# Optimization experiments

Hardware: AMD Instinct MI355X
Metric: run time of the kernel (lower is better)

Reference implementation:

```python
import jax, jax.numpy as jnp
import numpy as np
import itertools, math

METRIC = [1.0, 1.0, 1.0]  # Cl(3,0)
EPS = 1e-6
SQRT2 = math.sqrt(2.0)


def _build_algebra(metric):
    d = len(metric)
    # basis blades ordered by grade, then lexicographic combination (repo convention)
    blades = []
    for g in range(d + 1):
        for c in itertools.combinations(range(d), g):
            blades.append(sum(1 << i for i in c))
    idx = {m: i for i, m in enumerate(blades)}
    n = len(blades)
    C = np.zeros((n, n, n), dtype=np.float32)  # cayley[i, j, k]: e_i * e_k -> sign * e_j
    for ia, am in enumerate(blades):
        for ik, bm in enumerate(blades):
            a = am >> 1
            swaps = 0
            while a:
                swaps += bin(a & bm).count('1')
                a >>= 1
            sign = -1.0 if (swaps & 1) else 1.0
            for i in range(d):
                if am & bm & (1 << i):
                    sign *= metric[i]
            C[ia, idx[am ^ bm], ik] = sign
    grades = np.array([bin(m).count('1') for m in blades])
    subspaces = np.array([int((grades == g).sum()) for g in range(d + 1)])
    paths = np.zeros((d + 1, d + 1, d + 1), dtype=bool)
    for i in range(d + 1):
        for j in range(d + 1):
            for k in range(d + 1):
                paths[i, j, k] = np.any(C[np.ix_(grades == i, grades == j, grades == k)] != 0)
    return C, subspaces, paths, grades

CAYLEY_NP, SUBSPACES, PATHS, GRADE_OF_COMP = _build_algebra(METRIC)
REP_IDX = np.repeat(np.arange(len(SUBSPACES)), SUBSPACES)  # component -> grade, len 8
PI, PJ, PK = np.nonzero(PATHS)                              # 20 active grade triples
ONEHOT_GRADE = np.eye(len(SUBSPACES), dtype=np.float32)[GRADE_OF_COMP]  # [8,4]

B, N_IN, N_OUT = 1024, 256, 256
DIM_MV = CAYLEY_NP.shape[0]  # 8
N_PATHS = int(PATHS.sum())   # 20


def mv_linear(x, w, bias=None):
    # MVLinear: per-grade weight repeated over components; einsum 'bm...i,nmi->bn...i'
    wr = w[:, :, REP_IDX]                       # [out, in, 8]
    out = jnp.einsum('bmi,nmi->bni', x, wr)
    if bias is not None:
        out = out.at[:, :, 0].add(bias[:, :, 0])  # bias embedded in scalar (grade-0) slot
    return out


def normalize_mv(x, a):
    # per-grade norms (Euclidean metric => L2 norm of each grade block)
    oh = jnp.asarray(ONEHOT_GRADE)
    norms = jnp.sqrt(jnp.einsum('bni,ig->bng', x * x, oh))  # [b, n, 4]
    interp = jax.nn.sigmoid(a)[None] * (norms - 1.0) + 1.0  # learned interp toward unit norm
    return x / (interp[:, :, REP_IDX] + EPS)


def gp_kernel(gp_weight):
    # scatter 20 path weights into (m, n, 4, 4, 4), repeat per subspace, mask by cayley
    m, n, _ = gp_weight.shape
    g = len(SUBSPACES)
    w4 = jnp.zeros((m, n, g, g, g), gp_weight.dtype).at[:, :, PI, PJ, PK].set(gp_weight)
    wrep = w4[:, :, REP_IDX][:, :, :, REP_IDX][:, :, :, :, REP_IDX]  # [m, n, 8, 8, 8]
    return jnp.asarray(CAYLEY_NP)[None, None] * wrep


def setup_inputs() -> dict:
    key = jax.random.key(0)
    ks = jax.random.split(key, 5)
    std_gp = 1.0 / math.sqrt(N_IN * (len(METRIC) + 1))
    std_lin = 1.0 / math.sqrt(N_IN)
    return {
        'x': jax.random.normal(ks[0], (B, N_IN, DIM_MV), jnp.float32),
        'w_right': jax.random.normal(ks[1], (N_IN, N_IN, len(SUBSPACES)), jnp.float32) * std_lin,
        'w_left': jax.random.normal(ks[2], (N_OUT, N_IN, len(SUBSPACES)), jnp.float32) * std_lin,
        'b_left': jax.random.normal(ks[3], (1, N_OUT, 1), jnp.float32) * 0.02,
        'norm_a': jnp.zeros((N_IN, len(SUBSPACES)), jnp.float32),  # normalization_init = 0
        'gp_weight': jax.random.normal(ks[4], (N_OUT, N_IN, N_PATHS), jnp.float32) * std_gp,
    }


def reference(x, w_right, w_left, b_left, norm_a, gp_weight):
    x_right = normalize_mv(mv_linear(x, w_right), norm_a)
    kernel = gp_kernel(gp_weight)                 # [m, n, 8, 8, 8]
    outer = jnp.einsum('bni,bnk->bnik', x, x_right)  # [b, n, 8, 8]
    prod = jnp.einsum('bnik,mnijk->bmj', outer, kernel)
    left = mv_linear(x, w_left, b_left)
    return (left + prod) / SQRT2
```

## Files before the change

kernel.cpp:

```cpp
#include <hip/hip_runtime.h>
#include <math.h>

typedef unsigned short ushortT;
typedef __bf16 bf16x8 __attribute__((ext_vector_type(8)));
typedef float  f32x4  __attribute__((ext_vector_type(4)));

__constant__ int GRADEc[8] = {0,1,1,1,2,2,2,3};

__constant__ int CMAPc[8][7] = {
  {0, 8, 9,10,11, 0, 0},
  {1,12,13,14,15,16,17},
  {2,18,19,20,21,22,23},
  {3,24,25,26,27,28,29},
  {4,30,31,32,33,34,35},
  {5,36,37,38,39,40,41},
  {6,42,43,44,45,46,47},
  {7,48,49,50,51, 0, 0}};
__constant__ int WMAPc[8][7] = {
  {0, 4, 8,14,20, 0, 0},
  {1, 5, 9,10,15,16,21},
  {1, 5, 9,10,15,16,21},
  {1, 5, 9,10,15,16,21},
  {2, 6,11,12,17,18,22},
  {2, 6,11,12,17,18,22},
  {2, 6,11,12,17,18,22},
  {3, 7,13,19,23, 0, 0}};
__constant__ int SSTARTc[8][4] = {
  {0,2,3,4},{0,2,4,6},{0,2,4,6},{0,2,4,6},
  {0,2,4,6},{0,2,4,6},{0,2,4,6},{0,2,3,4}};
__constant__ int SCOUNTc[8][4] = {
  {2,1,1,1},{2,2,2,1},{2,2,2,1},{2,2,2,1},
  {2,2,2,1},{2,2,2,1},{2,2,2,1},{2,1,1,1}};

__device__ __forceinline__ ushortT f2bf(float f) {
  unsigned int u = __float_as_uint(f);
  unsigned int r = (u + 0x7fffu + ((u >> 16) & 1u)) >> 16;
  return (ushortT)r;
}

#define GLOAD_LDS16(gsrc, ldst) \
  __builtin_amdgcn_global_load_lds((const __attribute__((address_space(1))) unsigned int*)(gsrc), \
                                   (__attribute__((address_space(3))) unsigned int*)(ldst), 16, 0, 0)

__global__ void k_prep(const float* __restrict__ x, const float* __restrict__ w_right,
                       const float* __restrict__ w_left, const float* __restrict__ gp,
                       ushortT* __restrict__ XH, ushortT* __restrict__ XL,
                       ushortT* __restrict__ WH, ushortT* __restrict__ WL,
                       ushortT* __restrict__ WT2b) {
  const int bid = blockIdx.x;
  const int tid = threadIdx.x;
  if (bid < 6144) {
    int t = bid * 256 + tid;
    int n = t & 255, m = (t >> 8) & 255, w = t >> 16;
    float v = (w < 4) ? w_left[m * 1024 + n * 4 + w] : gp[m * 5120 + n * 20 + (w - 4)];
    WT2b[t] = f2bf(v);
  } else if (bid < 7168) {
    int b = bid - 6144;
    const float4* xp = (const float4*)(x + b * 2048 + tid * 8);
    float4 a = xp[0], c = xp[1];
    float v[8] = {a.x, a.y, a.z, a.w, c.x, c.y, c.z, c.w};
    #pragma unroll
    for (int i = 0; i < 8; ++i) {
      ushortT h = f2bf(v[i]);
      float hf = __uint_as_float(((unsigned int)h) << 16);
      XH[i * 262144 + b * 256 + tid] = h;
      XL[i * 262144 + b * 256 + tid] = f2bf(v[i] - hf);
    }
  } else {
    int n = bid - 7168;
    float4 w = *(const float4*)(w_right + n * 1024 + tid * 4);
    float v[4] = {w.x, w.y, w.z, w.w};
    #pragma unroll
    for (int g = 0; g < 4; ++g) {
      ushortT h = f2bf(v[g]);
      float hf = __uint_as_float(((unsigned int)h) << 16);
      WH[g * 65536 + n * 256 + tid] = h;
      WL[g * 65536 + n * 256 + tid] = f2bf(v[g] - hf);
    }
  }
}

__global__ __launch_bounds__(512) void k_right_feat(const ushortT* __restrict__ XH,
                                                    const ushortT* __restrict__ XL,
                                                    const ushortT* __restrict__ WH,
                                                    const ushortT* __restrict__ WL,
                                                    const float* __restrict__ x,
                                                    const float* __restrict__ norm_a,
                                                    ushortT* __restrict__ FT2b) {
  const int n0 = blockIdx.x * 32;
  const int b0 = blockIdx.y * 32;
  __shared__ __align__(16) ushortT lds[49152];
  const int t    = threadIdx.x;
  const int wave = t >> 6;
  const int lane = t & 63;
  const int i    = wave;
  const int g    = GRADEc[i];
  const int lrow = lane & 15, lkg = lane >> 4;
  const int srow = lane >> 2;
  const int sseg = lane & 3;

  const ushortT* Asrc_h = XH + i * 262144 + b0 * 256;
  const ushortT* Asrc_l = XL + i * 262144 + b0 * 256;
  const int bg = wave >> 1;
  const ushortT* Bsrc = ((wave & 1) ? WL : WH) + bg * 65536 + n0 * 256;

  f32x4 acc[2][2];
  #pragma unroll
  for (int r = 0; r < 2; ++r)
    #pragma unroll
    for (int c = 0; c < 2; ++c)
      acc[r][c] = (f32x4){0.f, 0.f, 0.f, 0.f};

  auto STAGE = [&](int k0, int buf) {
    ushortT* base = lds + buf * 24576;
    #pragma unroll
    for (int q = 0; q < 2; ++q) {
      int row = q * 16 + srow;
      int slog = sseg ^ ((row >> 1) & 3);
      GLOAD_LDS16(Asrc_h + row * 256 + k0 + slog * 8, base + i * 1024 + q * 512);
      GLOAD_LDS16(Asrc_l + row * 256 + k0 + slog * 8, base + 8192 + i * 1024 + q * 512);
      GLOAD_LDS16(Bsrc   + row * 256 + k0 + slog * 8,
                  base + 16384 + (wave & 1) * 4096 + bg * 1024 + q * 512);
    }
  };

  auto COMPUTE = [&](int buf) {
    const ushortT* base = lds + buf * 24576;
    bf16x8 afh[2], afl[2], bfh[2], bfl[2];
    #pragma unroll
    for (int r = 0; r < 2; ++r) {
      int row = r * 16 + lrow;
      int po = row * 32 + (lkg ^ ((row >> 1) & 3)) * 8;
      afh[r] = *(const bf16x8*)(base + i * 1024 + po);
      afl[r] = *(const bf16x8*)(base + 8192 + i * 1024 + po);
    }
    #pragma unroll
    for (int c = 0; c < 2; ++c) {
      int row = c * 16 + lrow;
      int po = row * 32 + (lkg ^ ((row >> 1) & 3)) * 8;
      bfh[c] = *(const bf16x8*)(base + 16384 + g * 1024 + po);
      bfl[c] = *(const bf16x8*)(base + 20480 + g * 1024 + po);
    }
    #pragma unroll
    for (int r = 0; r < 2; ++r)
      #pragma unroll
      for (int c = 0; c < 2; ++c) {
        acc[r][c] = __builtin_amdgcn_mfma_f32_16x16x32_bf16(afh[r], bfh[c], acc[r][c], 0, 0, 0);
        acc[r][c] = __builtin_amdgcn_mfma_f32_16x16x32_bf16(afl[r], bfh[c], acc[r][c], 0, 0, 0);
        acc[r][c] = __builtin_amdgcn_mfma_f32_16x16x32_bf16(afh[r], bfl[c], acc[r][c], 0, 0, 0);
      }
  };

  STAGE(0, 0);
  __syncthreads();
  int cur = 0;
  for (int tc = 0; tc < 8; ++tc) {
    if (tc < 7) STAGE((tc + 1) * 32, cur ^ 1);
    COMPUTE(cur);
    __syncthreads();
    cur ^= 1;
  }

  float* yl = (float*)lds;
  #pragma unroll
  for (int r = 0; r < 2; ++r)
    #pragma unroll
    for (int c = 0; c < 2; ++c)
      #pragma unroll
      for (int e = 0; e < 4; ++e) {
        int row = r * 16 + lkg * 4 + e;
        int col = c * 16 + lrow;
        yl[i * 1056 + row * 33 + col] = acc[r][c][e];
      }
  __syncthreads();

  #pragma unroll
  for (int e2 = 0; e2 < 2; ++e2) {
    int el  = t + e2 * 512;
    int row = el >> 5, col = el & 31;
    int b = b0 + row, n = n0 + col;
    float y[8];
    #pragma unroll
    for (int q = 0; q < 8; ++q) y[q] = yl[q * 1056 + row * 33 + col];
    const float4* xp = (const float4*)(x + b * 2048 + n * 8);
    float4 x01 = xp[0], x23 = xp[1];
    float xv[8] = {x01.x, x01.y, x01.z, x01.w, x23.x, x23.y, x23.z, x23.w};
    float4 na = *(const float4*)(norm_a + n * 4);
    float nav[4] = {na.x, na.y, na.z, na.w};
    float nr[4];
    nr[0] = fabsf(y[0]);
    nr[1] = sqrtf(y[1]*y[1] + y[2]*y[2] + y[3]*y[3]);
    nr[2] = sqrtf(y[4]*y[4] + y[5]*y[5] + y[6]*y[6]);
    nr[3] = fabsf(y[7]);
    float inv[4];
    #pragma unroll
    for (int gg = 0; gg < 4; ++gg) {
      float s = 1.0f / (1.0f + expf(-nav[gg]));
      inv[gg] = 1.0f / (s * (nr[gg] - 1.0f) + 1.0f + 1e-6f);
    }
    float r[8];
    r[0] = y[0]*inv[0];
    r[1] = y[1]*inv[1]; r[2] = y[2]*inv[1]; r[3] = y[3]*inv[1];
    r[4] = y[4]*inv[2]; r[5] = y[5]*inv[2]; r[6] = y[6]*inv[2];
    r[7] = y[7]*inv[3];

    float F[52];
    F[8]  = xv[0]*r[0];
    F[9]  = xv[1]*r[1] + xv[2]*r[2] + xv[3]*r[3];
    F[10] = -(xv[4]*r[4] + xv[5]*r[5] + xv[6]*r[6]);
    F[11] = -xv[7]*r[7];
    F[12] = xv[0]*r[1];
    F[13] = xv[1]*r[0];
    F[14] = -(xv[2]*r[4] + xv[3]*r[5]);
    F[15] = xv[4]*r[2] + xv[5]*r[3];
    F[16] = -xv[6]*r[7];
    F[17] = -xv[7]*r[6];
    F[18] = xv[0]*r[2];
    F[19] = xv[2]*r[0];
    F[20] = xv[1]*r[4] - xv[3]*r[6];
    F[21] = -xv[4]*r[1] + xv[6]*r[3];
    F[22] = xv[5]*r[7];
    F[23] = xv[7]*r[5];
    F[24] = xv[0]*r[3];
    F[25] = xv[3]*r[0];
    F[26] = xv[1]*r[5] + xv[2]*r[6];
    F[27] = -(xv[5]*r[1] + xv[6]*r[2]);
    F[28] = -xv[4]*r[7];
    F[29] = -xv[7]*r[4];
    F[30] = xv[0]*r[4];
    F[31] = xv[1]*r[2] - xv[2]*r[1];
    F[32] = xv[3]*r[7];
    F[33] = xv[4]*r[0];
    F[34] = -xv[5]*r[6] + xv[6]*r[5];
    F[35] = xv[7]*r[3];
    F[36] = xv[0]*r[5];
    F[37] = xv[1]*r[3] - xv[3]*r[1];
    F[38] = -xv[2]*r[7];
    F[39] = xv[5]*r[0];
    F[40] = xv[4]*r[6] - xv[6]*r[4];
    F[41] = -xv[7]*r[2];
    F[42] = xv[0]*r[6];
    F[43] = xv[2]*r[3] - xv[3]*r[2];
    F[44] = xv[1]*r[7];
    F[45] = xv[6]*r[0];
    F[46] = -xv[4]*r[5] + xv[5]*r[4];
    F[47] = xv[7]*r[1];
    F[48] = xv[0]*r[7];
    F[49] = xv[1]*r[6] - xv[2]*r[5] + xv[3]*r[4];
    F[50] = xv[4]*r[3] - xv[5]*r[2] + xv[6]*r[1];
    F[51] = xv[7]*r[0];

    #pragma unroll
    for (int c = 8; c < 52; ++c)
      FT2b[c * 262144 + b * 256 + n] = f2bf(F[c]);
  }
}

__global__ __launch_bounds__(256) void k_gemm_mfma(const ushortT* __restrict__ XH,
                                                   const ushortT* __restrict__ FT2b,
                                                   const ushortT* __restrict__ WT2b,
                                                   float* __restrict__ outP) {
  const int j  = blockIdx.z >> 2;
  const int ks = blockIdx.z & 3;
  const int b0 = blockIdx.y * 128;
  const int m0 = blockIdx.x * 128;
  __shared__ __align__(16) ushortT lds[32768];
  const int t    = threadIdx.x;
  const int wave = t >> 6;
  const int lane = t & 63;
  const int wb   = (wave & 1) * 64;
  const int wm   = (wave >> 1) * 64;
  const int lrow = lane & 15;
  const int lkg  = lane >> 4;
  const int srow = lane >> 3;
  const int sseg = lane & 7;

  f32x4 acc[4][4];
  #pragma unroll
  for (int r = 0; r < 4; ++r)
    #pragma unroll
    for (int c = 0; c < 4; ++c)
      acc[r][c] = (f32x4){0.f, 0.f, 0.f, 0.f};

  const int sstart = SSTARTc[j][ks];
  const int nt     = SCOUNTc[j][ks] * 4;

  auto STAGE = [&](int tch, int buf) {
    int slot = sstart + (tch >> 2);
    int k0   = (tch & 3) << 6;
    const ushortT* Ap = ((slot == 0) ? (XH + j * 262144)
                                     : (FT2b + CMAPc[j][slot] * 262144)) + b0 * 256;
    const ushortT* Bp = WT2b + WMAPc[j][slot] * 65536 + m0 * 256;
    #pragma unroll
    for (int q = 0; q < 4; ++q) {
      int idx = wave * 4 + q;
      int row = idx * 8 + srow;
      int slog = sseg ^ (row & 7);
      GLOAD_LDS16(Ap + row * 256 + k0 + slog * 8, lds + buf * 8192 + idx * 512);
      GLOAD_LDS16(Bp + row * 256 + k0 + slog * 8, lds + 16384 + buf * 8192 + idx * 512);
    }
  };

  STAGE(0, 0);
  __syncthreads();
  int cur = 0;
  for (int tc = 0; tc < nt; ++tc) {
    if (tc + 1 < nt) STAGE(tc + 1, cur ^ 1);
    const ushortT* sA = lds + cur * 8192;
    const ushortT* sB = lds + 16384 + cur * 8192;
    #pragma unroll
    for (int kk = 0; kk < 2; ++kk) {
      bf16x8 af[4], bf[4];
      #pragma unroll
      for (int r = 0; r < 4; ++r) {
        int row = wb + r * 16 + lrow;
        af[r] = *(const bf16x8*)(sA + row * 64 + (((kk * 4 + lkg) ^ (row & 7)) * 8));
      }
      #pragma unroll
      for (int c = 0; c < 4; ++c) {
        int row = wm + c * 16 + lrow;
        bf[c] = *(const bf16x8*)(sB + row * 64 + (((kk * 4 + lkg) ^ (row & 7)) * 8));
      }
      #pragma unroll
      for (int r = 0; r < 4; ++r)
        #pragma unroll
        for (int c = 0; c < 4; ++c)
          acc[r][c] = __builtin_amdgcn_mfma_f32_16x16x32_bf16(af[r], bf[c], acc[r][c], 0, 0, 0);
    }
    __syncthreads();
    cur ^= 1;
  }

  float* oj = outP + (ks * 8 + j) * 262144;
  #pragma unroll
  for (int r = 0; r < 4; ++r) {
    #pragma unroll
    for (int c = 0; c < 4; ++c) {
      #pragma unroll
      for (int e = 0; e < 4; ++e) {
        int brow = b0 + wb + r * 16 + lkg * 4 + e;
        int mcol = m0 + wm + c * 16 + lrow;
        oj[brow * 256 + mcol] = acc[r][c][e];
      }
    }
  }
}

__global__ void k_merge(const float* __restrict__ outP, const float* __restrict__ bleft,
                        float* __restrict__ out) {
  const int t4 = (blockIdx.x * 256 + threadIdx.x) * 4;
  const int m  = t4 & 255;
  const float sc = 0.7071067811865475f;
  float o[4][8];
  #pragma unroll
  for (int jj = 0; jj < 8; ++jj) {
    float4 s = make_float4(0.f, 0.f, 0.f, 0.f);
    #pragma unroll
    for (int p = 0; p < 4; ++p) {
      float4 v = *(const float4*)(outP + (p * 8 + jj) * 262144 + t4);
      s.x += v.x; s.y += v.y; s.z += v.z; s.w += v.w;
    }
    o[0][jj] = s.x; o[1][jj] = s.y; o[2][jj] = s.z; o[3][jj] = s.w;
  }
  #pragma unroll
  for (int q = 0; q < 4; ++q) {
    float ov[8];
    #pragma unroll
    for (int jj = 0; jj < 8; ++jj) ov[jj] = o[q][jj];
    ov[0] += bleft[m + q];
    float4 v0 = make_float4(ov[0]*sc, ov[1]*sc, ov[2]*sc, ov[3]*sc);
    float4 v1 = make_float4(ov[4]*sc, ov[5]*sc, ov[6]*sc, ov[7]*sc);
    *(float4*)(out + (t4 + q) * 8)     = v0;
    *(float4*)(out + (t4 + q) * 8 + 4) = v1;
  }
}

extern "C" void kernel_launch(void* const* d_in, const int* in_sizes, int n_in,
                              void* d_out, int out_size, void* d_ws, size_t ws_size,
                              hipStream_t stream) {
  const float* x       = (const float*)d_in[0];
  const float* w_right = (const float*)d_in[1];
  const float* w_left  = (const float*)d_in[2];
  const float* b_left  = (const float*)d_in[3];
  const float* norm_a  = (const float*)d_in[4];
  const float* gp      = (const float*)d_in[5];
  float* out = (float*)d_out;
  float* W   = (float*)d_ws;

  float*   outP = W;
  ushortT* XH   = (ushortT*)(W + 8388608);
  ushortT* XL   = (ushortT*)(W + 9437184);
  ushortT* WH   = (ushortT*)(W + 10485760);
  ushortT* WL   = (ushortT*)(W + 10616832);
  ushortT* FT2b = (ushortT*)(W + 10747904);
  ushortT* WT2b = (ushortT*)(W + 17563648);

  k_prep<<<7424, 256, 0, stream>>>(x, w_right, w_left, gp, XH, XL, WH, WL, WT2b);
  k_right_feat<<<dim3(8, 32), 512, 0, stream>>>(XH, XL, WH, WL, x, norm_a, FT2b);
  k_gemm_mfma<<<dim3(2, 8, 32), 256, 0, stream>>>(XH, FT2b, WT2b, outP);
  k_merge<<<256, 256, 0, stream>>>(outP, b_left, out);
}
```

Baseline: 123.2 us.

## Use partial vmcnt waits with raw barriers and remap block order for XCD locality

```diff
diff --git a/kernel.cpp b/kernel.cpp
--- a/kernel.cpp
+++ b/kernel.cpp
@@ -25,6 +25,7 @@
   {2, 6,11,12,17,18,22},
   {2, 6,11,12,17,18,22},
   {3, 7,13,19,23, 0, 0}};
+__constant__ int NSLOTc[8] = {5,7,7,7,7,7,7,5};
 __constant__ int SSTARTc[8][4] = {
   {0,2,3,4},{0,2,4,6},{0,2,4,6},{0,2,4,6},
   {0,2,4,6},{0,2,4,6},{0,2,4,6},{0,2,3,4}};
@@ -41,6 +42,10 @@
 #define GLOAD_LDS16(gsrc, ldst) \
   __builtin_amdgcn_global_load_lds((const __attribute__((address_space(1))) unsigned int*)(gsrc), \
                                    (__attribute__((address_space(3))) unsigned int*)(ldst), 16, 0, 0)
+
+#define WAITVM(N) asm volatile("s_waitcnt vmcnt(" #N ")" ::: "memory")
+#define SCHEDB()  __builtin_amdgcn_sched_barrier(0)
+#define RAWBAR()  do { SCHEDB(); __builtin_amdgcn_s_barrier(); asm volatile("" ::: "memory"); SCHEDB(); } while (0)
 
 __global__ void k_prep(const float* __restrict__ x, const float* __restrict__ w_right,
                        const float* __restrict__ w_left, const float* __restrict__ gp,
@@ -87,8 +92,13 @@
                                                     const float* __restrict__ x,
                                                     const float* __restrict__ norm_a,
                                                     ushortT* __restrict__ FT2b) {
-  const int n0 = blockIdx.x * 32;
-  const int b0 = blockIdx.y * 32;
+  const int lin = blockIdx.x;
+  const int rr  = lin & 7;
+  const int q   = lin >> 3;
+  const int xb  = q & 7;
+  const int yb  = (q >> 3) * 8 + rr;
+  const int n0 = xb * 32;
+  const int b0 = yb * 32;
   __shared__ __align__(16) ushortT lds[49152];
   const int t    = threadIdx.x;
   const int wave = t >> 6;
@@ -114,13 +124,13 @@
   auto STAGE = [&](int k0, int buf) {
     ushortT* base = lds + buf * 24576;
     #pragma unroll
-    for (int q = 0; q < 2; ++q) {
-      int row = q * 16 + srow;
+    for (int q2 = 0; q2 < 2; ++q2) {
+      int row = q2 * 16 + srow;
       int slog = sseg ^ ((row >> 1) & 3);
-      GLOAD_LDS16(Asrc_h + row * 256 + k0 + slog * 8, base + i * 1024 + q * 512);
-      GLOAD_LDS16(Asrc_l + row * 256 + k0 + slog * 8, base + 8192 + i * 1024 + q * 512);
+      GLOAD_LDS16(Asrc_h + row * 256 + k0 + slog * 8, base + i * 1024 + q2 * 512);
+      GLOAD_LDS16(Asrc_l + row * 256 + k0 + slog * 8, base + 8192 + i * 1024 + q2 * 512);
       GLOAD_LDS16(Bsrc   + row * 256 + k0 + slog * 8,
-                  base + 16384 + (wave & 1) * 4096 + bg * 1024 + q * 512);
+                  base + 16384 + (wave & 1) * 4096 + bg * 1024 + q2 * 512);
     }
   };
 
@@ -152,12 +162,13 @@
   };
 
   STAGE(0, 0);
-  __syncthreads();
   int cur = 0;
   for (int tc = 0; tc < 8; ++tc) {
-    if (tc < 7) STAGE((tc + 1) * 32, cur ^ 1);
+    if (tc < 7) { STAGE((tc + 1) * 32, cur ^ 1); SCHEDB(); WAITVM(6); }
+    else        { WAITVM(0); }
+    RAWBAR();
     COMPUTE(cur);
-    __syncthreads();
+    if (tc < 7) RAWBAR();
     cur ^= 1;
   }
 
@@ -181,7 +192,7 @@
     int b = b0 + row, n = n0 + col;
     float y[8];
     #pragma unroll
-    for (int q = 0; q < 8; ++q) y[q] = yl[q * 1056 + row * 33 + col];
+    for (int q2 = 0; q2 < 8; ++q2) y[q2] = yl[q2 * 1056 + row * 33 + col];
     const float4* xp = (const float4*)(x + b * 2048 + n * 8);
     float4 x01 = xp[0], x23 = xp[1];
     float xv[8] = {x01.x, x01.y, x01.z, x01.w, x23.x, x23.y, x23.z, x23.w};
@@ -260,10 +271,15 @@
                                                    const ushortT* __restrict__ FT2b,
                                                    const ushortT* __restrict__ WT2b,
                                                    float* __restrict__ outP) {
-  const int j  = blockIdx.z >> 2;
-  const int ks = blockIdx.z & 3;
-  const int b0 = blockIdx.y * 128;
-  const int m0 = blockIdx.x * 128;
+  const int lin = blockIdx.x;
+  const int rr  = lin & 7;
+  const int q   = lin >> 3;
+  const int ix  = q & 15;
+  const int z   = (q >> 4) * 8 + rr;
+  const int j   = z >> 2;
+  const int ks  = z & 3;
+  const int m0  = (ix & 1) * 128;
+  const int b0  = (ix >> 1) * 128;
   __shared__ __align__(16) ushortT lds[32768];
   const int t    = threadIdx.x;
   const int wave = t >> 6;
@@ -292,8 +308,8 @@
                                      : (FT2b + CMAPc[j][slot] * 262144)) + b0 * 256;
     const ushortT* Bp = WT2b + WMAPc[j][slot] * 65536 + m0 * 256;
     #pragma unroll
-    for (int q = 0; q < 4; ++q) {
-      int idx = wave * 4 + q;
+    for (int q2 = 0; q2 < 4; ++q2) {
+      int idx = wave * 4 + q2;
       int row = idx * 8 + srow;
       int slog = sseg ^ (row & 7);
       GLOAD_LDS16(Ap + row * 256 + k0 + slog * 8, lds + buf * 8192 + idx * 512);
@@ -302,10 +318,11 @@
   };
 
   STAGE(0, 0);
-  __syncthreads();
   int cur = 0;
   for (int tc = 0; tc < nt; ++tc) {
-    if (tc + 1 < nt) STAGE(tc + 1, cur ^ 1);
+    if (tc + 1 < nt) { STAGE(tc + 1, cur ^ 1); SCHEDB(); WAITVM(8); }
+    else             { WAITVM(0); }
+    RAWBAR();
     const ushortT* sA = lds + cur * 8192;
     const ushortT* sB = lds + 16384 + cur * 8192;
     #pragma unroll
@@ -327,7 +344,7 @@
         for (int c = 0; c < 4; ++c)
           acc[r][c] = __builtin_amdgcn_mfma_f32_16x16x32_bf16(af[r], bf[c], acc[r][c], 0, 0, 0);
     }
-    __syncthreads();
+    if (tc + 1 < nt) RAWBAR();
     cur ^= 1;
   }
 
@@ -396,7 +413,7 @@
   ushortT* WT2b = (ushortT*)(W + 17563648);
 
   k_prep<<<7424, 256, 0, stream>>>(x, w_right, w_left, gp, XH, XL, WH, WL, WT2b);
-  k_right_feat<<<dim3(8, 32), 512, 0, stream>>>(XH, XL, WH, WL, x, norm_a, FT2b);
-  k_gemm_mfma<<<dim3(2, 8, 32), 256, 0, stream>>>(XH, FT2b, WT2b, outP);
+  k_right_feat<<<256, 512, 0, stream>>>(XH, XL, WH, WL, x, norm_a, FT2b);
+  k_gemm_mfma<<<512, 256, 0, stream>>>(XH, FT2b, WT2b, outP);
   k_merge<<<256, 256, 0, stream>>>(outP, b_left, out);
 }
```

After: 116.5 us. 1.06x faster.
